# Optimization experiments

Measured on AMD Instinct MI355X. Metric: run time of the kernel, lower is better.

## Reference

```python
import jax, jax.numpy as jnp
import numpy as np

B, T, I = 32768, 28, 28
H, C = 128, 10


def setup_inputs() -> dict:
    key = jax.random.key(0)
    ks = jax.random.split(key, 7)
    s_u = 1.0 / np.sqrt(I)
    s_w = 1.0 / np.sqrt(H)
    return {
        "x": jax.random.normal(ks[0], (B, T, I), dtype=jnp.float32),
        "U_w": jax.random.uniform(ks[1], (H, I), jnp.float32, -s_u, s_u),
        "U_b": jax.random.uniform(ks[2], (H,), jnp.float32, -s_u, s_u),
        "W_w": jax.random.uniform(ks[3], (H, H), jnp.float32, -s_w, s_w),
        "W_b": jax.random.uniform(ks[4], (H,), jnp.float32, -s_w, s_w),
        "V_w": jax.random.uniform(ks[5], (C, H), jnp.float32, -s_w, s_w),
        "V_b": jax.random.uniform(ks[6], (C,), jnp.float32, -s_w, s_w),
    }


def reference(x, U_w, U_b, W_w, W_b, V_w, V_b):
    # x: [B, T, I]. Precompute input projections for all timesteps at once
    # (one big GEMM), then scan the sequential recurrence on S.
    ux = jnp.einsum("bti,hi->tbh", x, U_w) + U_b  # [T, B, H]

    def step(S, ux_t):
        S = jnp.tanh(ux_t + S @ W_w.T + W_b)
        return S, None

    S0 = jnp.zeros((x.shape[0], W_w.shape[0]), dtype=x.dtype)
    S_final, _ = jax.lax.scan(step, S0, ux)
    return S_final @ V_w.T + V_b  # [B, C]
```

## Files before the change

kernel.cpp:

```cpp
#include <hip/hip_runtime.h>


#define T_STEPS 28
#define I_DIM   28
#define S_STRIDE 136

typedef __attribute__((ext_vector_type(4))) float f32x4;
typedef __attribute__((ext_vector_type(8))) short short8;
typedef __attribute__((ext_vector_type(4))) unsigned int uint4v;

#define MFMA16 __builtin_amdgcn_mfma_f32_16x16x32_bf16

__device__ __forceinline__ unsigned pack2(float lo, float hi) {
#if __has_builtin(__builtin_amdgcn_cvt_pk_bf16_f32)
  auto p = __builtin_amdgcn_cvt_pk_bf16_f32(lo, hi);
  return __builtin_bit_cast(unsigned, p);
#else
  unsigned a = __builtin_bit_cast(unsigned, lo);
  a += 0x7FFFu + ((a >> 16) & 1u);
  unsigned b = __builtin_bit_cast(unsigned, hi);
  b += 0x7FFFu + ((b >> 16) & 1u);
  return (a >> 16) | (b & 0xFFFF0000u);
#endif
}

__device__ __forceinline__ float bf2f(unsigned short s) {
  return __builtin_bit_cast(float, (unsigned)s << 16);
}

__device__ __forceinline__ short8 to_frag(f32x4 a, f32x4 b) {
  union { unsigned u[4]; short8 v; } r;
  r.u[0] = pack2(a[0], a[1]);
  r.u[1] = pack2(a[2], a[3]);
  r.u[2] = pack2(b[0], b[1]);
  r.u[3] = pack2(b[2], b[3]);
  return r.v;
}

__device__ __forceinline__ short8 load_sfrag(const unsigned short* sp, int off) {
  uint4v d = *(const uint4v*)(sp + off);
  return __builtin_bit_cast(short8, d);
}

__device__ __forceinline__ f32x4 tanh4(f32x4 z) {
  f32x4 x2 = z * z;
  f32x4 p = 945.0f + x2 * (105.0f + x2);
  f32x4 q = 945.0f + x2 * (420.0f + 15.0f * x2);
  f32x4 num = z * p;
  f32x4 r;
#pragma unroll
  for (int i = 0; i < 4; ++i) r[i] = __builtin_amdgcn_rcpf(q[i]);
  f32x4 t = num * r;
#pragma unroll
  for (int i = 0; i < 4; ++i) t[i] = __builtin_amdgcn_fmed3f(t[i], -1.0f, 1.0f);
  return t;
}

__global__ __launch_bounds__(256, 4) void rnn_fused(
    const float* __restrict__ x,  const float* __restrict__ Uw,
    const float* __restrict__ Ub, const float* __restrict__ Ww,
    const float* __restrict__ Wb, const float* __restrict__ Vw,
    const float* __restrict__ Vb, float* __restrict__ out) {
  __shared__ __align__(16) unsigned short Sbuf[2][32 * S_STRIDE];

  const int tid  = threadIdx.x;
  const int w    = tid >> 6;
  const int lane = tid & 63;
  const int l15  = lane & 15;
  const int q    = lane >> 4;
  const int mrow = w * 32;
  const int b0   = blockIdx.x * 32;

  const f32x4 zero4 = {0.f, 0.f, 0.f, 0.f};

  short8 wfrag[2][4];
  short8 ufrag[2];
  f32x4  bias[2];
#pragma unroll
  for (int mt = 0; mt < 2; ++mt) {
    const int h = mrow + mt * 16 + l15;
    const float* wp = Ww + h * 128 + q * 8;
#pragma unroll
    for (int kt = 0; kt < 4; ++kt) {
      wfrag[mt][kt] = to_frag(*(const f32x4*)wp, *(const f32x4*)(wp + 4));
      wp += 32;
    }
    const float* up = Uw + h * I_DIM + q * 8;
    f32x4 u0 = *(const f32x4*)up;
    f32x4 u1 = zero4;
    if (q < 3) u1 = *(const f32x4*)(up + 4);
    ufrag[mt] = to_frag(u0, u1);
    const int hb = mrow + mt * 16 + q * 4;
    bias[mt] = *(const f32x4*)(Wb + hb) + *(const f32x4*)(Ub + hb);
  }

  const float* xlo[2];
  const float* xhi[2];
#pragma unroll
  for (int nt = 0; nt < 2; ++nt) {
    const float* base = x + (size_t)(b0 + nt * 16 + l15) * (T_STEPS * I_DIM);
    xlo[nt] = base + q * 8;
    xhi[nt] = base + ((q < 3) ? q * 8 + 4 : 0);
  }

  int ro[2];
#pragma unroll
  for (int nt = 0; nt < 2; ++nt) ro[nt] = (nt * 16 + l15) * S_STRIDE;

  f32x4 acc[2][2];
  short8 xf0, xf1;

  {
    f32x4 xa0 = *(const f32x4*)xlo[0], xb0 = *(const f32x4*)xhi[0];
    f32x4 xa1 = *(const f32x4*)xlo[1], xb1 = *(const f32x4*)xhi[1];
    xlo[0] += I_DIM; xhi[0] += I_DIM; xlo[1] += I_DIM; xhi[1] += I_DIM;
    f32x4 pa0 = *(const f32x4*)xlo[0], pb0 = *(const f32x4*)xhi[0];
    f32x4 pa1 = *(const f32x4*)xlo[1], pb1 = *(const f32x4*)xhi[1];

    xf0 = to_frag(xa0, xb0); xf1 = to_frag(xa1, xb1);
    unsigned short* wp = &Sbuf[1][0];
#pragma unroll
    for (int mt = 0; mt < 2; ++mt) {
      f32x4 d0 = MFMA16(ufrag[mt], xf0, bias[mt], 0, 0, 0);
      f32x4 d1 = MFMA16(ufrag[mt], xf1, bias[mt], 0, 0, 0);
      f32x4 t0 = tanh4(d0), t1 = tanh4(d1);
      uint2 dd0; dd0.x = pack2(t0[0], t0[1]); dd0.y = pack2(t0[2], t0[3]);
      uint2 dd1; dd1.x = pack2(t1[0], t1[1]); dd1.y = pack2(t1[2], t1[3]);
      *(uint2*)(wp + ro[0] + mrow + mt * 16 + q * 4) = dd0;
      *(uint2*)(wp + ro[1] + mrow + mt * 16 + q * 4) = dd1;
    }
    xf0 = to_frag(pa0, pb0); xf1 = to_frag(pa1, pb1);
  }
  __syncthreads();

#pragma unroll 1
  for (int t = 1; t < T_STEPS; ++t) {
    f32x4 pa0, pb0, pa1, pb1;
    const bool more = (t < T_STEPS - 1);
    if (more) {
      xlo[0] += I_DIM; xhi[0] += I_DIM; xlo[1] += I_DIM; xhi[1] += I_DIM;
      pa0 = *(const f32x4*)xlo[0]; pb0 = *(const f32x4*)xhi[0];
      pa1 = *(const f32x4*)xlo[1]; pb1 = *(const f32x4*)xhi[1];
    }

    const unsigned short* sp = &Sbuf[t & 1][0];

    short8 sA = load_sfrag(sp, ro[0] + q * 8);
    short8 sB = load_sfrag(sp, ro[1] + q * 8);
#pragma unroll
    for (int mt = 0; mt < 2; ++mt) {
      acc[mt][0] = MFMA16(wfrag[mt][0], sA, bias[mt], 0, 0, 0);
      acc[mt][1] = MFMA16(wfrag[mt][0], sB, bias[mt], 0, 0, 0);
    }
#pragma unroll
    for (int kt = 1; kt < 4; ++kt) {
      sA = load_sfrag(sp, ro[0] + kt * 32 + q * 8);
      sB = load_sfrag(sp, ro[1] + kt * 32 + q * 8);
#pragma unroll
      for (int mt = 0; mt < 2; ++mt) {
        acc[mt][0] = MFMA16(wfrag[mt][kt], sA, acc[mt][0], 0, 0, 0);
        acc[mt][1] = MFMA16(wfrag[mt][kt], sB, acc[mt][1], 0, 0, 0);
      }
    }
#pragma unroll
    for (int mt = 0; mt < 2; ++mt) {
      acc[mt][0] = MFMA16(ufrag[mt], xf0, acc[mt][0], 0, 0, 0);
      acc[mt][1] = MFMA16(ufrag[mt], xf1, acc[mt][1], 0, 0, 0);
    }

    unsigned short* wp = &Sbuf[(t + 1) & 1][0];
#pragma unroll
    for (int mt = 0; mt < 2; ++mt)
#pragma unroll
      for (int nt = 0; nt < 2; ++nt) {
        f32x4 th = tanh4(acc[mt][nt]);
        uint2 dd; dd.x = pack2(th[0], th[1]); dd.y = pack2(th[2], th[3]);
        *(uint2*)(wp + ro[nt] + mrow + mt * 16 + q * 4) = dd;
      }

    if (more) { xf0 = to_frag(pa0, pb0); xf1 = to_frag(pa1, pb1); }
    __syncthreads();
  }

  {
    const unsigned short* sf = &Sbuf[0][0];
    const int r  = tid >> 3;
    const int c0 = tid & 7;
    const float* v0 = Vw + c0 * 128;
    const float* v1 = Vw + ((c0 & 1) + 8) * 128;
    const unsigned short* srow = sf + r * S_STRIDE;
    float a0 = 0.f, a1 = 0.f;
#pragma unroll 8
    for (int h = 0; h < 128; ++h) {
      float s = bf2f(srow[h]);
      a0 += s * v0[h];
      a1 += s * v1[h];
    }
    float* op = out + (size_t)(b0 + r) * 10;
    op[c0] = a0 + Vb[c0];
    if (c0 < 2) op[c0 + 8] = a1 + Vb[(c0 & 1) + 8];
  }
}

extern "C" void kernel_launch(void* const* d_in, const int* in_sizes, int n_in,
                              void* d_out, int out_size, void* d_ws, size_t ws_size,
                              hipStream_t stream) {
  const float* x  = (const float*)d_in[0];
  const float* Uw = (const float*)d_in[1];
  const float* Ub = (const float*)d_in[2];
  const float* Ww = (const float*)d_in[3];
  const float* Wb = (const float*)d_in[4];
  const float* Vw = (const float*)d_in[5];
  const float* Vb = (const float*)d_in[6];
  rnn_fused<<<1024, 256, 0, stream>>>(x, Uw, Ub, Ww, Wb, Vw, Vb, (float*)d_out);
}
```

Baseline: 204.9 us.

## Stage x in LDS as bf16 chunks of seven timesteps with coalesced prefetch

Instead of each lane loading strided x rows from global memory every timestep, the block loads seven timesteps of its 32 rows with coalesced loads, converts them to bf16 and stores them in a shared buffer padded to 32 columns. The next chunk is prefetched into registers one step early and written at chunk boundaries, which costs an extra barrier there. The S buffer stride changes to 132 and fragment loads are split into two 64-bit reads, apparently to reduce LDS bank conflicts. The bf16 pack fallback switches to a cheaper round-half-up with a byte permute. Together these raise LDS and register use per block, which could lower occupancy.

```diff
diff --git a/kernel.cpp b/kernel.cpp
--- a/kernel.cpp
+++ b/kernel.cpp
@@ -2,12 +2,12 @@
 
 
 #define T_STEPS 28
-#define I_DIM   28
-#define S_STRIDE 136
+#define S_STRIDE 132
+#define X_STRIDE 228
+#define NSLOT 1568
 
 typedef __attribute__((ext_vector_type(4))) float f32x4;
 typedef __attribute__((ext_vector_type(8))) short short8;
-typedef __attribute__((ext_vector_type(4))) unsigned int uint4v;
 
 #define MFMA16 __builtin_amdgcn_mfma_f32_16x16x32_bf16
 
@@ -16,11 +16,9 @@
   auto p = __builtin_amdgcn_cvt_pk_bf16_f32(lo, hi);
   return __builtin_bit_cast(unsigned, p);
 #else
-  unsigned a = __builtin_bit_cast(unsigned, lo);
-  a += 0x7FFFu + ((a >> 16) & 1u);
-  unsigned b = __builtin_bit_cast(unsigned, hi);
-  b += 0x7FFFu + ((b >> 16) & 1u);
-  return (a >> 16) | (b & 0xFFFF0000u);
+  unsigned a = __builtin_bit_cast(unsigned, lo) + 0x8000u;
+  unsigned b = __builtin_bit_cast(unsigned, hi) + 0x8000u;
+  return __builtin_amdgcn_perm(b, a, 0x07060302u);
 #endif
 }
 
@@ -37,9 +35,11 @@
   return r.v;
 }
 
-__device__ __forceinline__ short8 load_sfrag(const unsigned short* sp, int off) {
-  uint4v d = *(const uint4v*)(sp + off);
-  return __builtin_bit_cast(short8, d);
+__device__ __forceinline__ short8 load_frag64(const unsigned short* sp, int off) {
+  union { uint2 d[2]; short8 v; } r;
+  r.d[0] = *(const uint2*)(sp + off);
+  r.d[1] = *(const uint2*)(sp + off + 4);
+  return r.v;
 }
 
 __device__ __forceinline__ f32x4 tanh4(f32x4 z) {
@@ -62,6 +62,7 @@
     const float* __restrict__ Wb, const float* __restrict__ Vw,
     const float* __restrict__ Vb, float* __restrict__ out) {
   __shared__ __align__(16) unsigned short Sbuf[2][32 * S_STRIDE];
+  __shared__ __align__(16) unsigned short Xbuf[32 * X_STRIDE];
 
   const int tid  = threadIdx.x;
   const int w    = tid >> 6;
@@ -85,7 +86,7 @@
       wfrag[mt][kt] = to_frag(*(const f32x4*)wp, *(const f32x4*)(wp + 4));
       wp += 32;
     }
-    const float* up = Uw + h * I_DIM + q * 8;
+    const float* up = Uw + h * 28 + q * 8;
     f32x4 u0 = *(const f32x4*)up;
     f32x4 u1 = zero4;
     if (q < 3) u1 = *(const f32x4*)(up + 4);
@@ -94,30 +95,47 @@
     bias[mt] = *(const f32x4*)(Wb + hb) + *(const f32x4*)(Ub + hb);
   }
 
-  const float* xlo[2];
-  const float* xhi[2];
+  const float* xblk = x + (size_t)b0 * 784;
+
+  {
+    f32x4 r[7];
+#pragma unroll
+    for (int k = 0; k < 7; ++k) {
+      int s = tid + 256 * k;
+      if (s < NSLOT) {
+        int row = s / 49, rem = s - row * 49, tl = rem / 7, g = rem - tl * 7;
+        r[k] = *(const f32x4*)(xblk + row * 784 + tl * 28 + g * 4);
+      }
+    }
+#pragma unroll
+    for (int k = 0; k < 7; ++k) {
+      int s = tid + 256 * k;
+      if (s < NSLOT) {
+        int row = s / 49, rem = s - row * 49, tl = rem / 7, g = rem - tl * 7;
+        uint2 d; d.x = pack2(r[k][0], r[k][1]); d.y = pack2(r[k][2], r[k][3]);
+        *(uint2*)(Xbuf + row * X_STRIDE + tl * 32 + g * 4) = d;
+        if (g == 0) {
+          uint2 zz; zz.x = 0u; zz.y = 0u;
+          *(uint2*)(Xbuf + row * X_STRIDE + tl * 32 + 28) = zz;
+        }
+      }
+    }
+  }
+  __syncthreads();
+
+  int ro[2], xo[2];
 #pragma unroll
   for (int nt = 0; nt < 2; ++nt) {
-    const float* base = x + (size_t)(b0 + nt * 16 + l15) * (T_STEPS * I_DIM);
-    xlo[nt] = base + q * 8;
-    xhi[nt] = base + ((q < 3) ? q * 8 + 4 : 0);
-  }
-
-  int ro[2];
-#pragma unroll
-  for (int nt = 0; nt < 2; ++nt) ro[nt] = (nt * 16 + l15) * S_STRIDE;
+    ro[nt] = (nt * 16 + l15) * S_STRIDE;
+    xo[nt] = (nt * 16 + l15) * X_STRIDE + q * 8;
+  }
 
   f32x4 acc[2][2];
-  short8 xf0, xf1;
+  f32x4 rpf[7];
 
   {
-    f32x4 xa0 = *(const f32x4*)xlo[0], xb0 = *(const f32x4*)xhi[0];
-    f32x4 xa1 = *(const f32x4*)xlo[1], xb1 = *(const f32x4*)xhi[1];
-    xlo[0] += I_DIM; xhi[0] += I_DIM; xlo[1] += I_DIM; xhi[1] += I_DIM;
-    f32x4 pa0 = *(const f32x4*)xlo[0], pb0 = *(const f32x4*)xhi[0];
-    f32x4 pa1 = *(const f32x4*)xlo[1], pb1 = *(const f32x4*)xhi[1];
-
-    xf0 = to_frag(xa0, xb0); xf1 = to_frag(xa1, xb1);
+    short8 xf0 = load_frag64(&Xbuf[0], xo[0]);
+    short8 xf1 = load_frag64(&Xbuf[0], xo[1]);
     unsigned short* wp = &Sbuf[1][0];
 #pragma unroll
     for (int mt = 0; mt < 2; ++mt) {
@@ -129,24 +147,50 @@
       *(uint2*)(wp + ro[0] + mrow + mt * 16 + q * 4) = dd0;
       *(uint2*)(wp + ro[1] + mrow + mt * 16 + q * 4) = dd1;
     }
-    xf0 = to_frag(pa0, pb0); xf1 = to_frag(pa1, pb1);
   }
   __syncthreads();
 
+  int tl = 0;
 #pragma unroll 1
   for (int t = 1; t < T_STEPS; ++t) {
-    f32x4 pa0, pb0, pa1, pb1;
-    const bool more = (t < T_STEPS - 1);
-    if (more) {
-      xlo[0] += I_DIM; xhi[0] += I_DIM; xlo[1] += I_DIM; xhi[1] += I_DIM;
-      pa0 = *(const f32x4*)xlo[0]; pb0 = *(const f32x4*)xhi[0];
-      pa1 = *(const f32x4*)xlo[1]; pb1 = *(const f32x4*)xhi[1];
-    }
+    if (t == 7 || t == 14 || t == 21) {
+#pragma unroll
+      for (int k = 0; k < 7; ++k) {
+        int s = tid + 256 * k;
+        if (s < NSLOT) {
+          int row = s / 49, rem = s - row * 49, tll = rem / 7, g = rem - tll * 7;
+          uint2 d; d.x = pack2(rpf[k][0], rpf[k][1]);
+          d.y = pack2(rpf[k][2], rpf[k][3]);
+          *(uint2*)(Xbuf + row * X_STRIDE + tll * 32 + g * 4) = d;
+        }
+      }
+      __syncthreads();
+      tl = 0;
+    } else {
+      ++tl;
+    }
+
+    if (t == 6 || t == 13 || t == 20) {
+      const int c = (t + 1) / 7;
+#pragma unroll
+      for (int k = 0; k < 7; ++k) {
+        int s = tid + 256 * k;
+        if (s < NSLOT) {
+          int row = s / 49, rem = s - row * 49, tll = rem / 7, g = rem - tll * 7;
+          rpf[k] = *(const f32x4*)(xblk + row * 784 + c * 196 + tll * 28 + g * 4);
+        }
+      }
+    }
+
+    short8 xf0 = load_frag64(&Xbuf[0], xo[0] + tl * 32);
+    short8 xf1 = load_frag64(&Xbuf[0], xo[1] + tl * 32);
 
     const unsigned short* sp = &Sbuf[t & 1][0];
-
-    short8 sA = load_sfrag(sp, ro[0] + q * 8);
-    short8 sB = load_sfrag(sp, ro[1] + q * 8);
+    const unsigned short* spA = sp + ro[0] + q * 8;
+    const unsigned short* spB = sp + ro[1] + q * 8;
+
+    short8 sA = load_frag64(spA, 0);
+    short8 sB = load_frag64(spB, 0);
 #pragma unroll
     for (int mt = 0; mt < 2; ++mt) {
       acc[mt][0] = MFMA16(wfrag[mt][0], sA, bias[mt], 0, 0, 0);
@@ -154,8 +198,8 @@
     }
 #pragma unroll
     for (int kt = 1; kt < 4; ++kt) {
-      sA = load_sfrag(sp, ro[0] + kt * 32 + q * 8);
-      sB = load_sfrag(sp, ro[1] + kt * 32 + q * 8);
+      sA = load_frag64(spA, kt * 32);
+      sB = load_frag64(spB, kt * 32);
 #pragma unroll
       for (int mt = 0; mt < 2; ++mt) {
         acc[mt][0] = MFMA16(wfrag[mt][kt], sA, acc[mt][0], 0, 0, 0);
@@ -177,8 +221,6 @@
         uint2 dd; dd.x = pack2(th[0], th[1]); dd.y = pack2(th[2], th[3]);
         *(uint2*)(wp + ro[nt] + mrow + mt * 16 + q * 4) = dd;
       }
-
-    if (more) { xf0 = to_frag(pa0, pb0); xf1 = to_frag(pa1, pb1); }
     __syncthreads();
   }
 
```

After: 229.9 us. 1.12x slower.

## Stage whole x tile into LDS as bf16 upfront, halve batch per block

Applied to the files above, without the earlier changes.

Each block now handles 16 batch rows instead of 32 and launches twice as many blocks. At kernel start the block's entire x slice (all 28 timesteps) is loaded with coalesced vector loads, converted to bf16 and stored in a padded LDS buffer, so the recurrence loop reads x fragments from LDS instead of issuing strided global loads every step. Row strides are changed to 132 and 900 to alter LDS bank mapping, and fragments are read with 64-bit LDS loads. In exchange, LDS use per block rises by about 29 KB, which may limit occupancy, and each wave's serial recurrence now does half the MFMA work per barrier.

```diff
diff --git a/kernel.cpp b/kernel.cpp
--- a/kernel.cpp
+++ b/kernel.cpp
@@ -2,12 +2,12 @@
 
 
 #define T_STEPS 28
-#define I_DIM   28
-#define S_STRIDE 136
+#define S_STRIDE 132
+#define X_STRIDE 900
+#define XSLOTS 3136
 
 typedef __attribute__((ext_vector_type(4))) float f32x4;
 typedef __attribute__((ext_vector_type(8))) short short8;
-typedef __attribute__((ext_vector_type(4))) unsigned int uint4v;
 
 #define MFMA16 __builtin_amdgcn_mfma_f32_16x16x32_bf16
 
@@ -37,9 +37,11 @@
   return r.v;
 }
 
-__device__ __forceinline__ short8 load_sfrag(const unsigned short* sp, int off) {
-  uint4v d = *(const uint4v*)(sp + off);
-  return __builtin_bit_cast(short8, d);
+__device__ __forceinline__ short8 load_frag64(const unsigned short* sp, int off) {
+  union { uint2 d[2]; short8 v; } r;
+  r.d[0] = *(const uint2*)(sp + off);
+  r.d[1] = *(const uint2*)(sp + off + 4);
+  return r.v;
 }
 
 __device__ __forceinline__ f32x4 tanh4(f32x4 z) {
@@ -61,7 +63,8 @@
     const float* __restrict__ Ub, const float* __restrict__ Ww,
     const float* __restrict__ Wb, const float* __restrict__ Vw,
     const float* __restrict__ Vb, float* __restrict__ out) {
-  __shared__ __align__(16) unsigned short Sbuf[2][32 * S_STRIDE];
+  __shared__ __align__(16) unsigned short Sbuf[2][16 * S_STRIDE];
+  __shared__ __align__(16) unsigned short Xbuf[16 * X_STRIDE];
 
   const int tid  = threadIdx.x;
   const int w    = tid >> 6;
@@ -69,9 +72,32 @@
   const int l15  = lane & 15;
   const int q    = lane >> 4;
   const int mrow = w * 32;
-  const int b0   = blockIdx.x * 32;
+  const int b0   = blockIdx.x * 16;
 
   const f32x4 zero4 = {0.f, 0.f, 0.f, 0.f};
+  const float* xblk = x + (size_t)b0 * 784;
+
+  {
+    f32x4 xr[13];
+#pragma unroll
+    for (int k = 0; k < 13; ++k) {
+      int s = tid + 256 * k;
+      if (s < XSLOTS) xr[k] = *(const f32x4*)(xblk + s * 4);
+    }
+#pragma unroll
+    for (int k = 0; k < 13; ++k) {
+      int s = tid + 256 * k;
+      if (s < XSLOTS) {
+        int row = s / 196, g = s - row * 196, tt = g / 7, j = g - tt * 7;
+        uint2 d; d.x = pack2(xr[k][0], xr[k][1]); d.y = pack2(xr[k][2], xr[k][3]);
+        *(uint2*)(Xbuf + row * X_STRIDE + tt * 32 + j * 4) = d;
+        if (j == 0) {
+          uint2 zz; zz.x = 0u; zz.y = 0u;
+          *(uint2*)(Xbuf + row * X_STRIDE + tt * 32 + 28) = zz;
+        }
+      }
+    }
+  }
 
   short8 wfrag[2][4];
   short8 ufrag[2];
@@ -85,7 +111,7 @@
       wfrag[mt][kt] = to_frag(*(const f32x4*)wp, *(const f32x4*)(wp + 4));
       wp += 32;
     }
-    const float* up = Uw + h * I_DIM + q * 8;
+    const float* up = Uw + h * 28 + q * 8;
     f32x4 u0 = *(const f32x4*)up;
     f32x4 u1 = zero4;
     if (q < 3) u1 = *(const f32x4*)(up + 4);
@@ -93,112 +119,67 @@
     const int hb = mrow + mt * 16 + q * 4;
     bias[mt] = *(const f32x4*)(Wb + hb) + *(const f32x4*)(Ub + hb);
   }
+  __syncthreads();
 
-  const float* xlo[2];
-  const float* xhi[2];
-#pragma unroll
-  for (int nt = 0; nt < 2; ++nt) {
-    const float* base = x + (size_t)(b0 + nt * 16 + l15) * (T_STEPS * I_DIM);
-    xlo[nt] = base + q * 8;
-    xhi[nt] = base + ((q < 3) ? q * 8 + 4 : 0);
-  }
-
-  int ro[2];
-#pragma unroll
-  for (int nt = 0; nt < 2; ++nt) ro[nt] = (nt * 16 + l15) * S_STRIDE;
-
-  f32x4 acc[2][2];
-  short8 xf0, xf1;
+  const int ro = l15 * S_STRIDE;
+  const int xo = l15 * X_STRIDE + q * 8;
+  f32x4 acc[2];
 
   {
-    f32x4 xa0 = *(const f32x4*)xlo[0], xb0 = *(const f32x4*)xhi[0];
-    f32x4 xa1 = *(const f32x4*)xlo[1], xb1 = *(const f32x4*)xhi[1];
-    xlo[0] += I_DIM; xhi[0] += I_DIM; xlo[1] += I_DIM; xhi[1] += I_DIM;
-    f32x4 pa0 = *(const f32x4*)xlo[0], pb0 = *(const f32x4*)xhi[0];
-    f32x4 pa1 = *(const f32x4*)xlo[1], pb1 = *(const f32x4*)xhi[1];
-
-    xf0 = to_frag(xa0, xb0); xf1 = to_frag(xa1, xb1);
+    short8 xf = load_frag64(&Xbuf[0], xo);
     unsigned short* wp = &Sbuf[1][0];
 #pragma unroll
     for (int mt = 0; mt < 2; ++mt) {
-      f32x4 d0 = MFMA16(ufrag[mt], xf0, bias[mt], 0, 0, 0);
-      f32x4 d1 = MFMA16(ufrag[mt], xf1, bias[mt], 0, 0, 0);
-      f32x4 t0 = tanh4(d0), t1 = tanh4(d1);
-      uint2 dd0; dd0.x = pack2(t0[0], t0[1]); dd0.y = pack2(t0[2], t0[3]);
-      uint2 dd1; dd1.x = pack2(t1[0], t1[1]); dd1.y = pack2(t1[2], t1[3]);
-      *(uint2*)(wp + ro[0] + mrow + mt * 16 + q * 4) = dd0;
-      *(uint2*)(wp + ro[1] + mrow + mt * 16 + q * 4) = dd1;
+      f32x4 d0 = MFMA16(ufrag[mt], xf, bias[mt], 0, 0, 0);
+      f32x4 t0 = tanh4(d0);
+      uint2 dd; dd.x = pack2(t0[0], t0[1]); dd.y = pack2(t0[2], t0[3]);
+      *(uint2*)(wp + ro + mrow + mt * 16 + q * 4) = dd;
     }
-    xf0 = to_frag(pa0, pb0); xf1 = to_frag(pa1, pb1);
   }
   __syncthreads();
 
 #pragma unroll 1
   for (int t = 1; t < T_STEPS; ++t) {
-    f32x4 pa0, pb0, pa1, pb1;
-    const bool more = (t < T_STEPS - 1);
-    if (more) {
-      xlo[0] += I_DIM; xhi[0] += I_DIM; xlo[1] += I_DIM; xhi[1] += I_DIM;
-      pa0 = *(const f32x4*)xlo[0]; pb0 = *(const f32x4*)xhi[0];
-      pa1 = *(const f32x4*)xlo[1]; pb1 = *(const f32x4*)xhi[1];
-    }
+    short8 xf = load_frag64(&Xbuf[0], xo + t * 32);
 
-    const unsigned short* sp = &Sbuf[t & 1][0];
+    const unsigned short* sp = &Sbuf[t & 1][0] + ro + q * 8;
 
-    short8 sA = load_sfrag(sp, ro[0] + q * 8);
-    short8 sB = load_sfrag(sp, ro[1] + q * 8);
+    short8 sA = load_frag64(sp, 0);
 #pragma unroll
-    for (int mt = 0; mt < 2; ++mt) {
-      acc[mt][0] = MFMA16(wfrag[mt][0], sA, bias[mt], 0, 0, 0);
-      acc[mt][1] = MFMA16(wfrag[mt][0], sB, bias[mt], 0, 0, 0);
+    for (int mt = 0; mt < 2; ++mt)
+      acc[mt] = MFMA16(wfrag[mt][0], sA, bias[mt], 0, 0, 0);
+#pragma unroll
+    for (int kt = 1; kt < 4; ++kt) {
+      sA = load_frag64(sp, kt * 32);
+#pragma unroll
+      for (int mt = 0; mt < 2; ++mt)
+        acc[mt] = MFMA16(wfrag[mt][kt], sA, acc[mt], 0, 0, 0);
     }
 #pragma unroll
-    for (int kt = 1; kt < 4; ++kt) {
-      sA = load_sfrag(sp, ro[0] + kt * 32 + q * 8);
-      sB = load_sfrag(sp, ro[1] + kt * 32 + q * 8);
-#pragma unroll
-      for (int mt = 0; mt < 2; ++mt) {
-        acc[mt][0] = MFMA16(wfrag[mt][kt], sA, acc[mt][0], 0, 0, 0);
-        acc[mt][1] = MFMA16(wfrag[mt][kt], sB, acc[mt][1], 0, 0, 0);
-      }
-    }
-#pragma unroll
-    for (int mt = 0; mt < 2; ++mt) {
-      acc[mt][0] = MFMA16(ufrag[mt], xf0, acc[mt][0], 0, 0, 0);
-      acc[mt][1] = MFMA16(ufrag[mt], xf1, acc[mt][1], 0, 0, 0);
-    }
+    for (int mt = 0; mt < 2; ++mt)
+      acc[mt] = MFMA16(ufrag[mt], xf, acc[mt], 0, 0, 0);
 
     unsigned short* wp = &Sbuf[(t + 1) & 1][0];
 #pragma unroll
-    for (int mt = 0; mt < 2; ++mt)
-#pragma unroll
-      for (int nt = 0; nt < 2; ++nt) {
-        f32x4 th = tanh4(acc[mt][nt]);
-        uint2 dd; dd.x = pack2(th[0], th[1]); dd.y = pack2(th[2], th[3]);
-        *(uint2*)(wp + ro[nt] + mrow + mt * 16 + q * 4) = dd;
-      }
-
-    if (more) { xf0 = to_frag(pa0, pb0); xf1 = to_frag(pa1, pb1); }
+    for (int mt = 0; mt < 2; ++mt) {
+      f32x4 th = tanh4(acc[mt]);
+      uint2 dd; dd.x = pack2(th[0], th[1]); dd.y = pack2(th[2], th[3]);
+      *(uint2*)(wp + ro + mrow + mt * 16 + q * 4) = dd;
+    }
     __syncthreads();
   }
 
   {
-    const unsigned short* sf = &Sbuf[0][0];
-    const int r  = tid >> 3;
-    const int c0 = tid & 7;
-    const float* v0 = Vw + c0 * 128;
-    const float* v1 = Vw + ((c0 & 1) + 8) * 128;
-    const unsigned short* srow = sf + r * S_STRIDE;
-    float a0 = 0.f, a1 = 0.f;
+    const int r  = tid >> 4;
+    const int c0 = tid & 15;
+    if (c0 < 10) {
+      const float* v0 = Vw + c0 * 128;
+      const unsigned short* srow = &Sbuf[0][0] + r * S_STRIDE;
+      float a0 = 0.f;
 #pragma unroll 8
-    for (int h = 0; h < 128; ++h) {
-      float s = bf2f(srow[h]);
-      a0 += s * v0[h];
-      a1 += s * v1[h];
+      for (int h = 0; h < 128; ++h) a0 += bf2f(srow[h]) * v0[h];
+      out[(size_t)(b0 + r) * 10 + c0] = a0 + Vb[c0];
     }
-    float* op = out + (size_t)(b0 + r) * 10;
-    op[c0] = a0 + Vb[c0];
-    if (c0 < 2) op[c0 + 8] = a1 + Vb[(c0 & 1) + 8];
   }
 }
 
@@ -212,5 +193,5 @@
   const float* Wb = (const float*)d_in[4];
   const float* Vw = (const float*)d_in[5];
   const float* Vb = (const float*)d_in[6];
-  rnn_fused<<<1024, 256, 0, stream>>>(x, Uw, Ub, Ww, Wb, Vw, Vb, (float*)d_out);
+  rnn_fused<<<2048, 256, 0, stream>>>(x, Uw, Ub, Ww, Wb, Vw, Vb, (float*)d_out);
 }
```

New measurement: 200.3 us. 1.02x faster.
